# Optimization experiments

Measured on AMD Instinct MI355X. Metric: run time of the kernel, lower is better.

Reference implementation:

```python
import jax, jax.numpy as jnp
import numpy as np

MIN_GAP = 5
MIN_SIZE = 5
# max_size defaults to inf, so the upper bound min(i+MAX_SIZE, T) is just T


def setup_inputs() -> dict:
    key = jax.random.key(0)
    k1, k2 = jax.random.split(key)
    B, T = 8, 4096
    w_phi = jax.random.normal(k1, (B, 1, T), dtype=jnp.float32)
    # target onset/offset frame indices in [0, T)
    y = jax.random.uniform(k2, (B, 2), dtype=jnp.float32) * T
    return {"w_phi": w_phi, "y": y, "eps": 5}


def reference(w_phi, y, eps):
    B, _, T = w_phi.shape
    x = w_phi[:, 0, :]  # [B, T] per-frame scores
    idx = jnp.arange(T, dtype=x.dtype)
    # hinge penalties: max(0, |y0 - i| - eps), max(0, |y1 - j| - eps)
    pi = jnp.maximum(0.0, jnp.abs(y[:, 0:1] - idx) - eps)  # [B, T]
    pj = jnp.maximum(0.0, jnp.abs(y[:, 1:2] - idx) - eps)  # [B, T]
    # score(i, j) = x[i] + x[j] + (pi[i] + pj[j]) / 2 = a[i] + b[j]
    a = x + 0.5 * pi  # onset part
    b = x + 0.5 * pj  # offset part
    ii = jnp.arange(T)
    # valid pairs: i >= MIN_GAP and j >= i + MIN_SIZE (j < T implicit)
    mask = (ii[:, None] >= MIN_GAP) & (ii[None, :] >= ii[:, None] + MIN_SIZE)
    scores = a[:, :, None] + b[:, None, :]  # [B, T, T]
    neg = jnp.finfo(scores.dtype).min
    best = jnp.max(jnp.where(mask[None], scores, neg), axis=(1, 2))  # [B]
    # initial candidate: onset=1, offset=1+MIN_SIZE (kept if strictly greatest)
    init = a[:, 1] + b[:, 1 + MIN_SIZE]
    out = jnp.maximum(best, init)
    return jnp.mean(out)  # loss summed over batch / batch_size
```

## Files before the change

kernel.cpp:

```cpp
#include <hip/hip_runtime.h>

#define T 4096
#define NTHREADS 1024
#define ELEMS_PER_THREAD 4
#define MIN_GAP 5
#define MIN_SIZE 5

__global__ __launch_bounds__(NTHREADS)
void custom_loss_kernel(const float* __restrict__ w_phi,
                        const float* __restrict__ y,
                        const int* __restrict__ eps_p,
                        float* __restrict__ out) {
    const int b = blockIdx.x;
    const int t = threadIdx.x;
    const float eps = (float)eps_p[0];
    const float y0 = y[b * 2 + 0];
    const float y1 = y[b * 2 + 1];
    const float* __restrict__ x = w_phi + (size_t)b * T;

    __shared__ float sm[T];
    __shared__ float wred[16];

    float a_loc[ELEMS_PER_THREAD];
    #pragma unroll
    for (int k = 0; k < ELEMS_PER_THREAD; k++) {
        int i = t + k * NTHREADS;
        float xi = x[i];
        float fi = (float)i;
        float pi = fmaxf(0.0f, fabsf(y0 - fi) - eps);
        float pj = fmaxf(0.0f, fabsf(y1 - fi) - eps);
        a_loc[k] = xi + 0.5f * pi;
        sm[i]    = xi + 0.5f * pj;
    }
    __syncthreads();

    for (int off = 1; off < T; off <<= 1) {
        float v[ELEMS_PER_THREAD];
        #pragma unroll
        for (int k = 0; k < ELEMS_PER_THREAD; k++) {
            int i = t + k * NTHREADS;
            float cur = sm[i];
            int j = i + off;
            if (j < T) cur = fmaxf(cur, sm[j]);
            v[k] = cur;
        }
        __syncthreads();
        #pragma unroll
        for (int k = 0; k < ELEMS_PER_THREAD; k++) {
            sm[t + k * NTHREADS] = v[k];
        }
        __syncthreads();
    }

    float best = -3.402823466e38f;
    #pragma unroll
    for (int k = 0; k < ELEMS_PER_THREAD; k++) {
        int i = t + k * NTHREADS;
        if (i >= MIN_GAP && (i + MIN_SIZE) < T) {
            best = fmaxf(best, a_loc[k] + sm[i + MIN_SIZE]);
        }
    }

    const int lane = t & 63;
    const int wid  = t >> 6;
    #pragma unroll
    for (int off = 32; off > 0; off >>= 1) {
        best = fmaxf(best, __shfl_down(best, off, 64));
    }
    if (lane == 0) wred[wid] = best;
    __syncthreads();

    if (wid == 0) {
        float v = (lane < (NTHREADS / 64)) ? wred[lane] : -3.402823466e38f;
        #pragma unroll
        for (int off = 8; off > 0; off >>= 1) {
            v = fmaxf(v, __shfl_down(v, off, 64));
        }
        if (lane == 0) {
            float a1 = x[1] + 0.5f * fmaxf(0.0f, fabsf(y0 - 1.0f) - eps);
            float b6 = x[6] + 0.5f * fmaxf(0.0f, fabsf(y1 - (float)(1 + MIN_SIZE)) - eps);
            float res = fmaxf(v, a1 + b6);
            atomicAdd(out, res * 0.125f);
        }
    }
}

extern "C" void kernel_launch(void* const* d_in, const int* in_sizes, int n_in,
                              void* d_out, int out_size, void* d_ws, size_t ws_size,
                              hipStream_t stream) {
    const float* w_phi = (const float*)d_in[0];
    const float* y     = (const float*)d_in[1];
    const int*   eps   = (const int*)d_in[2];
    float* out = (float*)d_out;

    hipMemsetAsync(out, 0, sizeof(float), stream);
    custom_loss_kernel<<<8, NTHREADS, 0, stream>>>(w_phi, y, eps, out);
}
```

Baseline: 62.01 us.

## Replace shared-memory doubling suffix-max with per-wave register scan in one block

Each batch row is now handled by one 64-lane wave. Every lane holds a contiguous chunk of 64 values in registers, computes a local suffix max, and combines chunks with a wave-shuffle scan. This removes the log2(T)-step shared-memory doubling loop and its many block barriers. The memset and atomicAdd are also dropped: a single 512-thread block writes the mean directly. The trade-off is heavy register pressure from the 64-element arrays and only one block on the GPU.

```diff
diff --git a/kernel.cpp b/kernel.cpp
--- a/kernel.cpp
+++ b/kernel.cpp
@@ -1,87 +1,102 @@
 #include <hip/hip_runtime.h>
 
 #define T 4096
-#define NTHREADS 1024
-#define ELEMS_PER_THREAD 4
+#define B 8
+#define CHUNK 64
 #define MIN_GAP 5
 #define MIN_SIZE 5
+#define NEG (-3.402823466e38f)
 
-__global__ __launch_bounds__(NTHREADS)
+__global__ __launch_bounds__(512, 2)
 void custom_loss_kernel(const float* __restrict__ w_phi,
                         const float* __restrict__ y,
                         const int* __restrict__ eps_p,
                         float* __restrict__ out) {
-    const int b = blockIdx.x;
-    const int t = threadIdx.x;
+    const int t    = threadIdx.x;
+    const int wave = t >> 6;
+    const int lane = t & 63;
+
     const float eps = (float)eps_p[0];
-    const float y0 = y[b * 2 + 0];
-    const float y1 = y[b * 2 + 1];
-    const float* __restrict__ x = w_phi + (size_t)b * T;
+    const float y0  = y[wave * 2 + 0];
+    const float y1  = y[wave * 2 + 1];
+    const float* __restrict__ x = w_phi + (size_t)wave * T + (size_t)lane * CHUNK;
 
-    __shared__ float sm[T];
-    __shared__ float wred[16];
+    __shared__ float wred[B];
 
-    float a_loc[ELEMS_PER_THREAD];
+    float xr[CHUNK];
     #pragma unroll
-    for (int k = 0; k < ELEMS_PER_THREAD; k++) {
-        int i = t + k * NTHREADS;
-        float xi = x[i];
-        float fi = (float)i;
-        float pi = fmaxf(0.0f, fabsf(y0 - fi) - eps);
-        float pj = fmaxf(0.0f, fabsf(y1 - fi) - eps);
-        a_loc[k] = xi + 0.5f * pi;
-        sm[i]    = xi + 0.5f * pj;
-    }
-    __syncthreads();
-
-    for (int off = 1; off < T; off <<= 1) {
-        float v[ELEMS_PER_THREAD];
-        #pragma unroll
-        for (int k = 0; k < ELEMS_PER_THREAD; k++) {
-            int i = t + k * NTHREADS;
-            float cur = sm[i];
-            int j = i + off;
-            if (j < T) cur = fmaxf(cur, sm[j]);
-            v[k] = cur;
-        }
-        __syncthreads();
-        #pragma unroll
-        for (int k = 0; k < ELEMS_PER_THREAD; k++) {
-            sm[t + k * NTHREADS] = v[k];
-        }
-        __syncthreads();
+    for (int q = 0; q < CHUNK / 4; q++) {
+        float4 v = ((const float4*)x)[q];
+        xr[4 * q + 0] = v.x;
+        xr[4 * q + 1] = v.y;
+        xr[4 * q + 2] = v.z;
+        xr[4 * q + 3] = v.w;
     }
 
-    float best = -3.402823466e38f;
-    #pragma unroll
-    for (int k = 0; k < ELEMS_PER_THREAD; k++) {
-        int i = t + k * NTHREADS;
-        if (i >= MIN_GAP && (i + MIN_SIZE) < T) {
-            best = fmaxf(best, a_loc[k] + sm[i + MIN_SIZE]);
+    const float base = (float)(lane * CHUNK);
+
+    float ls[CHUNK];
+    {
+        float run = NEG;
+        #pragma unroll
+        for (int j = CHUNK - 1; j >= 0; j--) {
+            float fj = base + (float)j;
+            float bj = xr[j] + 0.5f * fmaxf(0.0f, fabsf(y1 - fj) - eps);
+            run = fmaxf(run, bj);
+            ls[j] = run;
         }
     }
 
-    const int lane = t & 63;
-    const int wid  = t >> 6;
+    float inc = ls[0];
+    #pragma unroll
+    for (int off = 1; off < 64; off <<= 1) {
+        float u = __shfl_down(inc, off, 64);
+        inc = (lane + off < 64) ? fmaxf(inc, u) : inc;
+    }
+    float S = __shfl_down(inc, 1, 64);
+    if (lane == 63) S = NEG;
+
+    float nsm[MIN_SIZE];
+    #pragma unroll
+    for (int k = 0; k < MIN_SIZE; k++) {
+        nsm[k] = __shfl_down(fmaxf(ls[k], S), 1, 64);
+    }
+
+    float best = NEG;
+    #pragma unroll
+    for (int j = 0; j < CHUNK; j++) {
+        float fj = base + (float)j;
+        float aj = xr[j] + 0.5f * fmaxf(0.0f, fabsf(y0 - fj) - eps);
+        float smv;
+        bool valid;
+        if (j <= CHUNK - 1 - MIN_SIZE) {
+            smv   = fmaxf(ls[j + MIN_SIZE], S);
+            valid = true;
+        } else {
+            smv   = nsm[j - (CHUNK - MIN_SIZE)];
+            valid = (lane < 63);
+        }
+        if (lane == 0 && j < MIN_GAP) valid = false;
+        if (valid) best = fmaxf(best, aj + smv);
+    }
+
     #pragma unroll
     for (int off = 32; off > 0; off >>= 1) {
         best = fmaxf(best, __shfl_down(best, off, 64));
     }
-    if (lane == 0) wred[wid] = best;
+
+    if (lane == 0) {
+        float a1 = xr[1] + 0.5f * fmaxf(0.0f, fabsf(y0 - 1.0f) - eps);
+        float b6 = xr[6] + 0.5f * fmaxf(0.0f, fabsf(y1 - (float)(1 + MIN_SIZE)) - eps);
+        wred[wave] = fmaxf(best, a1 + b6);
+    }
     __syncthreads();
 
-    if (wid == 0) {
-        float v = (lane < (NTHREADS / 64)) ? wred[lane] : -3.402823466e38f;
+    if (t == 0) {
+        float s = 0.0f;
         #pragma unroll
-        for (int off = 8; off > 0; off >>= 1) {
-            v = fmaxf(v, __shfl_down(v, off, 64));
-        }
-        if (lane == 0) {
-            float a1 = x[1] + 0.5f * fmaxf(0.0f, fabsf(y0 - 1.0f) - eps);
-            float b6 = x[6] + 0.5f * fmaxf(0.0f, fabsf(y1 - (float)(1 + MIN_SIZE)) - eps);
-            float res = fmaxf(v, a1 + b6);
-            atomicAdd(out, res * 0.125f);
-        }
+        for (int k = 0; k < B; k++) s += wred[k];
+        out[0] = s * 0.125f;
     }
 }
 
@@ -93,6 +108,5 @@
     const int*   eps   = (const int*)d_in[2];
     float* out = (float*)d_out;
 
-    hipMemsetAsync(out, 0, sizeof(float), stream);
-    custom_loss_kernel<<<8, NTHREADS, 0, stream>>>(w_phi, y, eps, out);
+    custom_loss_kernel<<<1, 512, 0, stream>>>(w_phi, y, eps, out);
 }
```

New measurement: 60.71 us. 1.02x faster.
